# Performance work log

Measured on AMD Instinct MI355X. Metric: run time of the kernel, lower is better.

## Reference

```python
import jax, jax.numpy as jnp
import numpy as np

NB, M, FIN = 8, 32768, 32       # batch, mesh vertices, input features
RANK, FILT = 5, 32              # Chebyshev order, output filters
E = 262144                      # nnz of rescaled Laplacian (~8 per row)


def setup_inputs() -> dict:
    key = jax.random.key(0)
    ks = jax.random.split(key, 6)
    x = jax.random.normal(ks[0], (NB, M, FIN), dtype=jnp.float32)
    rows = jax.random.randint(ks[1], (E,), 0, M, dtype=jnp.int32)
    cols = jax.random.randint(ks[2], (E,), 0, M, dtype=jnp.int32)
    # rescaled-Laplacian values, roughly spectral-normalized
    vals = jax.random.normal(ks[3], (E,), dtype=jnp.float32) * np.float32(1.0 / np.sqrt(8.0))
    kernel = jax.random.normal(ks[4], (FIN * RANK, FILT), dtype=jnp.float32) * np.float32(0.05)
    bias = jnp.zeros((FILT,), dtype=jnp.float32)
    return {"x": x, "vals": vals, "kernel": kernel, "bias": bias, "rows": rows, "cols": cols}


def _spmm(rows, cols, vals, x0):
    # y[m, f, n] = sum_j L[m, j] * x0[j, f, n]   (COO SpMM via gather + segment_sum)
    g = vals[:, None, None] * x0[cols]           # [E, Fin, N]
    return jax.ops.segment_sum(g, rows, num_segments=x0.shape[0])


def reference(x, vals, kernel, bias, rows, cols):
    N, Mm, Fin = x.shape
    x0 = jnp.transpose(x, (1, 2, 0))             # [M, Fin, N]
    xs = [x0]
    x1 = x0
    if RANK > 1:
        x1 = _spmm(rows, cols, vals, x0)         # T_1 = L x
        xs.append(x1)
    for _ in range(2, RANK):                     # T_k = 2 L T_{k-1} - T_{k-2}
        x2 = 2.0 * _spmm(rows, cols, vals, x1) - x0
        xs.append(x2)
        x0, x1 = x1, x2
    xk = jnp.stack(xs, axis=0)                   # [K, M, Fin, N]
    xk = jnp.transpose(xk, (3, 1, 2, 0)).reshape(N * Mm, Fin * RANK)  # Fin-major, rank inner
    out = xk @ kernel + bias                     # [N*M, FILT]
    return out.reshape(N, Mm, FILT)
```

## Files before the change

kernel.cpp:

```cpp
#include <hip/hip_runtime.h>

#define M_VERT 32768
#define NBATCH 8
#define FIN 32
#define RANK 5
#define FILT 32
#define E_NNZ 262144
#define ROWLEN 256
#define EVROW 40

typedef short short8 __attribute__((ext_vector_type(8)));
typedef float f32x4 __attribute__((ext_vector_type(4)));

__device__ __forceinline__ float bfl(unsigned int u) {
    unsigned int x = u << 16; return __builtin_bit_cast(float, x);
}
__device__ __forceinline__ float bfh(unsigned int u) {
    unsigned int x = u & 0xffff0000u; return __builtin_bit_cast(float, x);
}
__device__ __forceinline__ unsigned int f2bf(float f) {
    unsigned int x = __builtin_bit_cast(unsigned int, f);
    return (x + 0x7fffu + ((x >> 16) & 1u)) >> 16;
}
__device__ __forceinline__ unsigned int pk(float a, float b) {
    return f2bf(a) | (f2bf(b) << 16);
}


__global__ void pack_kernel(const float* __restrict__ x, unsigned short* __restrict__ T0,
                            const int* __restrict__ rows, const int* __restrict__ cols,
                            const float* __restrict__ vals,
                            int* __restrict__ fill, int2* __restrict__ ev,
                            const float* __restrict__ W, unsigned short* __restrict__ Wb) {
    int tid = blockIdx.x * blockDim.x + threadIdx.x;
    int m = tid >> 5;
    int r = tid & 31;
    int n = r >> 2;
    int q = r & 3;
    const float* src = x + ((size_t)n * M_VERT + m) * FIN + q * 8;
    float4 v0 = *(const float4*)(src);
    float4 v1 = *(const float4*)(src + 4);
    uint4 u;
    u.x = pk(v0.x, v0.y); u.y = pk(v0.z, v0.w);
    u.z = pk(v1.x, v1.y); u.w = pk(v1.z, v1.w);
    *(uint4*)(T0 + (size_t)m * ROWLEN + n * FIN + q * 8) = u;

    if (tid < E_NNZ) {
        int rr = rows[tid];
        int pos = atomicAdd(&fill[rr], 1);
        if (pos < EVROW) {
            int2 p; p.x = cols[tid]; p.y = __builtin_bit_cast(int, vals[tid]);
            ev[rr * EVROW + pos] = p;
        }
    }

    if (tid < 640) {
        int lane = tid & 63;
        int kf = tid >> 6;
        int k = kf >> 1, ft = kf & 1;
        int f = ft * 16 + (lane & 15);
        int fin0 = (lane >> 4) * 8;
        unsigned short tmp[8];
#pragma unroll
        for (int j = 0; j < 8; ++j)
            tmp[j] = (unsigned short)f2bf(W[((fin0 + j) * RANK + k) * FILT + f]);
        uint4 uw;
        uw.x = (unsigned int)tmp[0] | ((unsigned int)tmp[1] << 16);
        uw.y = (unsigned int)tmp[2] | ((unsigned int)tmp[3] << 16);
        uw.z = (unsigned int)tmp[4] | ((unsigned int)tmp[5] << 16);
        uw.w = (unsigned int)tmp[6] | ((unsigned int)tmp[7] << 16);
        *(uint4*)(Wb + (size_t)tid * 8) = uw;
    }
}


__global__ __launch_bounds__(256) void spmm_kernel(const int* __restrict__ cnt,
                                                   const unsigned long long* __restrict__ ev,
                                                   const unsigned short* __restrict__ Tin,
                                                   const unsigned short* __restrict__ Tsub,
                                                   unsigned short* __restrict__ Tout, int cheb) {
    int w = threadIdx.x >> 6;
    int l = threadIdx.x & 63;
    int m = blockIdx.x * 4 + w;
    unsigned int coff = (unsigned int)l * 8u;
    int c = __builtin_amdgcn_readfirstlane(cnt[m]);
    int cp = (c + 7) & ~7;
    if (cp > EVROW) cp = EVROW;
    int s = m * EVROW;
    int e = s + cp;
    const char* tb = (const char*)Tin;
    float a0 = 0.f, a1 = 0.f, a2 = 0.f, a3 = 0.f;
    for (int j = s; j < e; j += 8) {
        unsigned long long ed[8];
#pragma unroll
        for (int i = 0; i < 8; ++i) ed[i] = ev[j + i];
        uint2 t[8];
#pragma unroll
        for (int i = 0; i < 8; ++i)
            t[i] = *(const uint2*)(tb + (((unsigned int)ed[i]) << 9) + coff);
#pragma unroll
        for (int i = 0; i < 8; ++i) {
            float v = __builtin_bit_cast(float, (unsigned int)(ed[i] >> 32));
            a0 += v * bfl(t[i].x); a1 += v * bfh(t[i].x);
            a2 += v * bfl(t[i].y); a3 += v * bfh(t[i].y);
        }
    }
    size_t moff = (size_t)m * 512 + coff;
    if (cheb) {
        unsigned long long o = __builtin_nontemporal_load(
            (const unsigned long long*)((const char*)Tsub + moff));
        unsigned int ox = (unsigned int)o, oy = (unsigned int)(o >> 32);
        a0 = 2.f * a0 - bfl(ox); a1 = 2.f * a1 - bfh(ox);
        a2 = 2.f * a2 - bfl(oy); a3 = 2.f * a3 - bfh(oy);
    }
    uint2 r;
    r.x = pk(a0, a1); r.y = pk(a2, a3);
    *(uint2*)((char*)Tout + moff) = r;
}


__global__ __launch_bounds__(256) void gemm_kernel(const unsigned short* __restrict__ T0,
                                                   const unsigned short* __restrict__ T1,
                                                   const unsigned short* __restrict__ T2,
                                                   const unsigned short* __restrict__ T3,
                                                   const unsigned short* __restrict__ T4,
                                                   const unsigned short* __restrict__ Wb,
                                                   const float* __restrict__ bias,
                                                   float* __restrict__ out) {
    int w = threadIdx.x >> 6;
    int l = threadIdx.x & 63;
    int n  = blockIdx.x & 7;
    int mb = blockIdx.x >> 3;
    int m0 = (mb * 4 + w) * 16;
    int lrow = l & 15;
    int quad = l >> 4;

    short8 bfrag[5][2];
#pragma unroll
    for (int kf = 0; kf < 10; ++kf)
        bfrag[kf >> 1][kf & 1] = *(const short8*)(Wb + ((size_t)kf * 64 + l) * 8);

    float b0 = bias[lrow];
    float b1 = bias[16 + lrow];

    const unsigned short* Ts[5] = {T0, T1, T2, T3, T4};
    size_t abase = (size_t)(m0 + lrow) * ROWLEN + quad * 8 + n * FIN;

    f32x4 c0 = {0.f, 0.f, 0.f, 0.f};
    f32x4 c1 = {0.f, 0.f, 0.f, 0.f};
#pragma unroll
    for (int k = 0; k < 5; ++k) {
        short8 a = *(const short8*)(Ts[k] + abase);
        c0 = __builtin_amdgcn_mfma_f32_16x16x32_bf16(a, bfrag[k][0], c0, 0, 0, 0);
        c1 = __builtin_amdgcn_mfma_f32_16x16x32_bf16(a, bfrag[k][1], c1, 0, 0, 0);
    }
    float* op = out + ((size_t)n * M_VERT + m0) * FILT;
#pragma unroll
    for (int r = 0; r < 4; ++r) {
        int orow = quad * 4 + r;
        __builtin_nontemporal_store(c0[r] + b0, &op[(size_t)orow * FILT + lrow]);
        __builtin_nontemporal_store(c1[r] + b1, &op[(size_t)orow * FILT + 16 + lrow]);
    }
}


extern "C" void kernel_launch(void* const* d_in, const int* in_sizes, int n_in,
                              void* d_out, int out_size, void* d_ws, size_t ws_size,
                              hipStream_t stream) {
    const float* x    = (const float*)d_in[0];
    const float* vals = (const float*)d_in[1];
    const float* W    = (const float*)d_in[2];
    const float* bias = (const float*)d_in[3];
    const int*   rows = (const int*)d_in[4];
    const int*   cols = (const int*)d_in[5];
    float* out = (float*)d_out;

    const size_t TSZ = (size_t)M_VERT * ROWLEN;
    unsigned short* T0 = (unsigned short*)d_ws;
    unsigned short* T1 = T0 + TSZ;
    unsigned short* T2 = T1 + TSZ;
    unsigned short* T3 = T2 + TSZ;
    unsigned short* T4 = T3 + TSZ;
    int*  fill = (int*)(T4 + TSZ);
    int2* ev   = (int2*)(fill + M_VERT);
    unsigned short* Wb = (unsigned short*)(ev + (size_t)M_VERT * EVROW);

    hipMemsetAsync(fill, 0, M_VERT * sizeof(int), stream);
    hipMemsetAsync(ev, 0, (size_t)M_VERT * EVROW * sizeof(int2), stream);
    pack_kernel<<<M_VERT * 32 / 256, 256, 0, stream>>>(x, T0, rows, cols, vals,
                                                       fill, ev, W, Wb);

    const unsigned long long* evq = (const unsigned long long*)ev;
    spmm_kernel<<<M_VERT / 4, 256, 0, stream>>>(fill, evq, T0, T0, T1, 0);
    spmm_kernel<<<M_VERT / 4, 256, 0, stream>>>(fill, evq, T1, T0, T2, 1);
    spmm_kernel<<<M_VERT / 4, 256, 0, stream>>>(fill, evq, T2, T1, T3, 1);
    spmm_kernel<<<M_VERT / 4, 256, 0, stream>>>(fill, evq, T3, T2, T4, 1);

    gemm_kernel<<<(M_VERT / 64) * 8, 256, 0, stream>>>(T0, T1, T2, T3, T4, Wb, bias, out);
}
```

Before: 231.4 us.

## Split Chebyshev tensors per batch and stage edge lists in LDS

Changes the T buffers from vertex-major rows holding all 8 batches [M][N*Fin] to batch-major [N][M][Fin]. Each SpMM block now handles 16 vertices for one batch, so each batch slice (2 MB of bf16) can stay cache-resident while neighbour rows are gathered. Edge lists are staged in shared memory once per block, and the loop runs to the exact count instead of padding to a multiple of 8, which lets the memset of the edge buffer be dropped. In exchange, each gather is now a 4-byte load per lane with 16-lane groups instead of an 8-byte load across a full wave, and edge lists are re-read once per batch.

```diff
diff --git a/kernel.cpp b/kernel.cpp
--- a/kernel.cpp
+++ b/kernel.cpp
@@ -33,17 +33,16 @@
                             int* __restrict__ fill, int2* __restrict__ ev,
                             const float* __restrict__ W, unsigned short* __restrict__ Wb) {
     int tid = blockIdx.x * blockDim.x + threadIdx.x;
-    int m = tid >> 5;
-    int r = tid & 31;
-    int n = r >> 2;
-    int q = r & 3;
+    int q = tid & 3;
+    int m = (tid >> 2) & (M_VERT - 1);
+    int n = tid >> 17;
     const float* src = x + ((size_t)n * M_VERT + m) * FIN + q * 8;
     float4 v0 = *(const float4*)(src);
     float4 v1 = *(const float4*)(src + 4);
     uint4 u;
     u.x = pk(v0.x, v0.y); u.y = pk(v0.z, v0.w);
     u.z = pk(v1.x, v1.y); u.w = pk(v1.z, v1.w);
-    *(uint4*)(T0 + (size_t)m * ROWLEN + n * FIN + q * 8) = u;
+    *(uint4*)(T0 + ((size_t)n * M_VERT + m) * 32 + q * 8) = u;
 
     if (tid < E_NNZ) {
         int rr = rows[tid];
@@ -79,43 +78,43 @@
                                                    const unsigned short* __restrict__ Tin,
                                                    const unsigned short* __restrict__ Tsub,
                                                    unsigned short* __restrict__ Tout, int cheb) {
-    int w = threadIdx.x >> 6;
-    int l = threadIdx.x & 63;
-    int m = blockIdx.x * 4 + w;
-    unsigned int coff = (unsigned int)l * 8u;
-    int c = __builtin_amdgcn_readfirstlane(cnt[m]);
-    int cp = (c + 7) & ~7;
-    if (cp > EVROW) cp = EVROW;
-    int s = m * EVROW;
-    int e = s + cp;
-    const char* tb = (const char*)Tin;
-    float a0 = 0.f, a1 = 0.f, a2 = 0.f, a3 = 0.f;
-    for (int j = s; j < e; j += 8) {
-        unsigned long long ed[8];
-#pragma unroll
-        for (int i = 0; i < 8; ++i) ed[i] = ev[j + i];
-        uint2 t[8];
-#pragma unroll
-        for (int i = 0; i < 8; ++i)
-            t[i] = *(const uint2*)(tb + (((unsigned int)ed[i]) << 9) + coff);
-#pragma unroll
-        for (int i = 0; i < 8; ++i) {
-            float v = __builtin_bit_cast(float, (unsigned int)(ed[i] >> 32));
-            a0 += v * bfl(t[i].x); a1 += v * bfh(t[i].x);
-            a2 += v * bfl(t[i].y); a3 += v * bfh(t[i].y);
-        }
+    __shared__ unsigned long long sev[16 * EVROW];
+    int n  = blockIdx.x & 7;
+    int vb = blockIdx.x >> 3;
+    int m0 = vb * 16;
+    int t  = threadIdx.x;
+
+    const unsigned long long* eb = ev + (size_t)m0 * EVROW;
+    for (int i = t; i < 16 * EVROW; i += 256)
+        sev[i] = __builtin_nontemporal_load(eb + i);
+
+    int g  = t >> 4;
+    int lq = t & 15;
+    int m  = m0 + g;
+    int c  = cnt[m];
+    if (c > EVROW) c = EVROW;
+    __syncthreads();
+
+    const char* sb = (const char*)Tin + ((size_t)n << 21);
+    unsigned int kof = (unsigned int)lq * 4u;
+    const unsigned long long* evg = sev + g * EVROW;
+    float a0 = 0.f, a1 = 0.f;
+    for (int j = 0; j < c; ++j) {
+        unsigned long long ed = evg[j];
+        unsigned int col = (unsigned int)ed;
+        float v = __builtin_bit_cast(float, (unsigned int)(ed >> 32));
+        unsigned int tv = *(const unsigned int*)(sb + (col << 6) + kof);
+        a0 += v * bfl(tv);
+        a1 += v * bfh(tv);
     }
-    size_t moff = (size_t)m * 512 + coff;
+    size_t moff = ((size_t)n << 21) + (((size_t)(unsigned int)m << 6) + kof);
     if (cheb) {
-        unsigned long long o = __builtin_nontemporal_load(
-            (const unsigned long long*)((const char*)Tsub + moff));
-        unsigned int ox = (unsigned int)o, oy = (unsigned int)(o >> 32);
-        a0 = 2.f * a0 - bfl(ox); a1 = 2.f * a1 - bfh(ox);
-        a2 = 2.f * a2 - bfl(oy); a3 = 2.f * a3 - bfh(oy);
+        unsigned int o = __builtin_nontemporal_load(
+            (const unsigned int*)((const char*)Tsub + moff));
+        a0 = 2.f * a0 - bfl(o);
+        a1 = 2.f * a1 - bfh(o);
     }
-    uint2 r;
-    r.x = pk(a0, a1); r.y = pk(a2, a3);
-    *(uint2*)((char*)Tout + moff) = r;
+    *(unsigned int*)((char*)Tout + moff) = pk(a0, a1);
 }
 
 
@@ -144,7 +143,7 @@
     float b1 = bias[16 + lrow];
 
     const unsigned short* Ts[5] = {T0, T1, T2, T3, T4};
-    size_t abase = (size_t)(m0 + lrow) * ROWLEN + quad * 8 + n * FIN;
+    size_t abase = ((size_t)n * M_VERT + (m0 + lrow)) * 32 + quad * 8;
 
     f32x4 c0 = {0.f, 0.f, 0.f, 0.f};
     f32x4 c1 = {0.f, 0.f, 0.f, 0.f};
@@ -186,15 +185,14 @@
     unsigned short* Wb = (unsigned short*)(ev + (size_t)M_VERT * EVROW);
 
     hipMemsetAsync(fill, 0, M_VERT * sizeof(int), stream);
-    hipMemsetAsync(ev, 0, (size_t)M_VERT * EVROW * sizeof(int2), stream);
     pack_kernel<<<M_VERT * 32 / 256, 256, 0, stream>>>(x, T0, rows, cols, vals,
                                                        fill, ev, W, Wb);
 
     const unsigned long long* evq = (const unsigned long long*)ev;
-    spmm_kernel<<<M_VERT / 4, 256, 0, stream>>>(fill, evq, T0, T0, T1, 0);
-    spmm_kernel<<<M_VERT / 4, 256, 0, stream>>>(fill, evq, T1, T0, T2, 1);
-    spmm_kernel<<<M_VERT / 4, 256, 0, stream>>>(fill, evq, T2, T1, T3, 1);
-    spmm_kernel<<<M_VERT / 4, 256, 0, stream>>>(fill, evq, T3, T2, T4, 1);
+    spmm_kernel<<<(M_VERT / 16) * 8, 256, 0, stream>>>(fill, evq, T0, T0, T1, 0);
+    spmm_kernel<<<(M_VERT / 16) * 8, 256, 0, stream>>>(fill, evq, T1, T0, T2, 1);
+    spmm_kernel<<<(M_VERT / 16) * 8, 256, 0, stream>>>(fill, evq, T2, T1, T3, 1);
+    spmm_kernel<<<(M_VERT / 16) * 8, 256, 0, stream>>>(fill, evq, T3, T2, T4, 1);
 
     gemm_kernel<<<(M_VERT / 64) * 8, 256, 0, stream>>>(T0, T1, T2, T3, T4, Wb, bias, out);
 }
```

Result: slower. 341.2 us (+47.4%).

## Fuse pack, SpMM chain and GEMM into one cooperative persistent kernel

Applied to the files above, without the earlier changes.

Replaces the two memsets and six separate kernel launches with a single cooperative kernel using grid-stride persistent loops and grid.sync between stages, sized from occupancy (up to 6 blocks per CU on 256 CUs). It aims to remove per-launch overhead and the tail drain between the dependent Chebyshev steps. In exchange, each stage runs on a capped persistent grid, and grid-wide barriers carry their own cost. The old multi-kernel path stays as a fallback if the cooperative launch fails.

```diff
diff --git a/kernel.cpp b/kernel.cpp
--- a/kernel.cpp
+++ b/kernel.cpp
@@ -1,4 +1,7 @@
 #include <hip/hip_runtime.h>
+#include <hip/hip_cooperative_groups.h>
+
+namespace cg = cooperative_groups;
 
 #define M_VERT 32768
 #define NBATCH 8
@@ -27,97 +30,204 @@
 }
 
 
-__global__ void pack_kernel(const float* __restrict__ x, unsigned short* __restrict__ T0,
-                            const int* __restrict__ rows, const int* __restrict__ cols,
-                            const float* __restrict__ vals,
-                            int* __restrict__ fill, int2* __restrict__ ev,
-                            const float* __restrict__ W, unsigned short* __restrict__ Wb) {
-    int tid = blockIdx.x * blockDim.x + threadIdx.x;
-    int m = tid >> 5;
-    int r = tid & 31;
-    int n = r >> 2;
-    int q = r & 3;
-    const float* src = x + ((size_t)n * M_VERT + m) * FIN + q * 8;
-    float4 v0 = *(const float4*)(src);
-    float4 v1 = *(const float4*)(src + 4);
-    uint4 u;
-    u.x = pk(v0.x, v0.y); u.y = pk(v0.z, v0.w);
-    u.z = pk(v1.x, v1.y); u.w = pk(v1.z, v1.w);
-    *(uint4*)(T0 + (size_t)m * ROWLEN + n * FIN + q * 8) = u;
-
-    if (tid < E_NNZ) {
-        int rr = rows[tid];
-        int pos = atomicAdd(&fill[rr], 1);
-        if (pos < EVROW) {
-            int2 p; p.x = cols[tid]; p.y = __builtin_bit_cast(int, vals[tid]);
-            ev[rr * EVROW + pos] = p;
-        }
-    }
-
-    if (tid < 640) {
-        int lane = tid & 63;
-        int kf = tid >> 6;
-        int k = kf >> 1, ft = kf & 1;
-        int f = ft * 16 + (lane & 15);
-        int fin0 = (lane >> 4) * 8;
-        unsigned short tmp[8];
-#pragma unroll
-        for (int j = 0; j < 8; ++j)
-            tmp[j] = (unsigned short)f2bf(W[((fin0 + j) * RANK + k) * FILT + f]);
-        uint4 uw;
-        uw.x = (unsigned int)tmp[0] | ((unsigned int)tmp[1] << 16);
-        uw.y = (unsigned int)tmp[2] | ((unsigned int)tmp[3] << 16);
-        uw.z = (unsigned int)tmp[4] | ((unsigned int)tmp[5] << 16);
-        uw.w = (unsigned int)tmp[6] | ((unsigned int)tmp[7] << 16);
-        *(uint4*)(Wb + (size_t)tid * 8) = uw;
-    }
-}
-
+__device__ __forceinline__ void pack_body(int G, const float* __restrict__ x,
+                                          unsigned short* __restrict__ T0,
+                                          const int* __restrict__ rows,
+                                          const int* __restrict__ cols,
+                                          const float* __restrict__ vals,
+                                          int* __restrict__ fill, int2* __restrict__ ev,
+                                          const float* __restrict__ W,
+                                          unsigned short* __restrict__ Wb) {
+    for (int tid = blockIdx.x * 256 + threadIdx.x; tid < M_VERT * 32; tid += G * 256) {
+        int m = tid >> 5;
+        int r = tid & 31;
+        int n = r >> 2;
+        int q = r & 3;
+        const float* src = x + ((size_t)n * M_VERT + m) * FIN + q * 8;
+        float4 v0 = *(const float4*)(src);
+        float4 v1 = *(const float4*)(src + 4);
+        uint4 u;
+        u.x = pk(v0.x, v0.y); u.y = pk(v0.z, v0.w);
+        u.z = pk(v1.x, v1.y); u.w = pk(v1.z, v1.w);
+        *(uint4*)(T0 + (size_t)m * ROWLEN + n * FIN + q * 8) = u;
+
+        if (tid < E_NNZ) {
+            int rr = rows[tid];
+            int pos = atomicAdd(&fill[rr], 1);
+            if (pos < EVROW) {
+                int2 p; p.x = cols[tid]; p.y = __builtin_bit_cast(int, vals[tid]);
+                ev[rr * EVROW + pos] = p;
+            }
+        }
+
+        if (tid < 640) {
+            int lane = tid & 63;
+            int kf = tid >> 6;
+            int k = kf >> 1, ft = kf & 1;
+            int f = ft * 16 + (lane & 15);
+            int fin0 = (lane >> 4) * 8;
+            unsigned short tmp[8];
+#pragma unroll
+            for (int j = 0; j < 8; ++j)
+                tmp[j] = (unsigned short)f2bf(W[((fin0 + j) * RANK + k) * FILT + f]);
+            uint4 uw;
+            uw.x = (unsigned int)tmp[0] | ((unsigned int)tmp[1] << 16);
+            uw.y = (unsigned int)tmp[2] | ((unsigned int)tmp[3] << 16);
+            uw.z = (unsigned int)tmp[4] | ((unsigned int)tmp[5] << 16);
+            uw.w = (unsigned int)tmp[6] | ((unsigned int)tmp[7] << 16);
+            *(uint4*)(Wb + (size_t)tid * 8) = uw;
+        }
+    }
+}
+
+__device__ __forceinline__ void spmm_body(int G, const int* __restrict__ cnt,
+                                          const unsigned long long* __restrict__ ev,
+                                          const unsigned short* __restrict__ Tin,
+                                          const unsigned short* __restrict__ Tsub,
+                                          unsigned short* __restrict__ Tout, int cheb) {
+    int w = threadIdx.x >> 6;
+    int l = threadIdx.x & 63;
+    unsigned int coff = (unsigned int)l * 8u;
+    const char* tb = (const char*)Tin;
+    for (int bv = blockIdx.x; bv < M_VERT / 4; bv += G) {
+        int m = bv * 4 + w;
+        int c = __builtin_amdgcn_readfirstlane(cnt[m]);
+        int cp = (c + 7) & ~7;
+        if (cp > EVROW) cp = EVROW;
+        int s = m * EVROW;
+        int e = s + cp;
+        float a0 = 0.f, a1 = 0.f, a2 = 0.f, a3 = 0.f;
+        for (int j = s; j < e; j += 8) {
+            unsigned long long ed[8];
+#pragma unroll
+            for (int i = 0; i < 8; ++i) ed[i] = ev[j + i];
+            uint2 t[8];
+#pragma unroll
+            for (int i = 0; i < 8; ++i)
+                t[i] = *(const uint2*)(tb + (((unsigned int)ed[i]) << 9) + coff);
+#pragma unroll
+            for (int i = 0; i < 8; ++i) {
+                float v = __builtin_bit_cast(float, (unsigned int)(ed[i] >> 32));
+                a0 += v * bfl(t[i].x); a1 += v * bfh(t[i].x);
+                a2 += v * bfl(t[i].y); a3 += v * bfh(t[i].y);
+            }
+        }
+        size_t moff = (size_t)m * 512 + coff;
+        if (cheb) {
+            unsigned long long o = __builtin_nontemporal_load(
+                (const unsigned long long*)((const char*)Tsub + moff));
+            unsigned int ox = (unsigned int)o, oy = (unsigned int)(o >> 32);
+            a0 = 2.f * a0 - bfl(ox); a1 = 2.f * a1 - bfh(ox);
+            a2 = 2.f * a2 - bfl(oy); a3 = 2.f * a3 - bfh(oy);
+        }
+        uint2 rr;
+        rr.x = pk(a0, a1); rr.y = pk(a2, a3);
+        *(uint2*)((char*)Tout + moff) = rr;
+    }
+}
+
+__device__ __forceinline__ void gemm_body(int G,
+                                          const unsigned short* __restrict__ T0,
+                                          const unsigned short* __restrict__ T1,
+                                          const unsigned short* __restrict__ T2,
+                                          const unsigned short* __restrict__ T3,
+                                          const unsigned short* __restrict__ T4,
+                                          const unsigned short* __restrict__ Wb,
+                                          const float* __restrict__ bias,
+                                          float* __restrict__ out) {
+    int w = threadIdx.x >> 6;
+    int l = threadIdx.x & 63;
+    int lrow = l & 15;
+    int quad = l >> 4;
+
+    short8 bfrag[5][2];
+#pragma unroll
+    for (int kf = 0; kf < 10; ++kf)
+        bfrag[kf >> 1][kf & 1] = *(const short8*)(Wb + ((size_t)kf * 64 + l) * 8);
+    float b0 = bias[lrow];
+    float b1 = bias[16 + lrow];
+    const unsigned short* Ts[5] = {T0, T1, T2, T3, T4};
+
+    for (int bv = blockIdx.x; bv < (M_VERT / 64) * 8; bv += G) {
+        int n  = bv & 7;
+        int mb = bv >> 3;
+        int m0 = (mb * 4 + w) * 16;
+        size_t abase = (size_t)(m0 + lrow) * ROWLEN + quad * 8 + n * FIN;
+        f32x4 c0 = {0.f, 0.f, 0.f, 0.f};
+        f32x4 c1 = {0.f, 0.f, 0.f, 0.f};
+#pragma unroll
+        for (int k = 0; k < 5; ++k) {
+            short8 a = *(const short8*)(Ts[k] + abase);
+            c0 = __builtin_amdgcn_mfma_f32_16x16x32_bf16(a, bfrag[k][0], c0, 0, 0, 0);
+            c1 = __builtin_amdgcn_mfma_f32_16x16x32_bf16(a, bfrag[k][1], c1, 0, 0, 0);
+        }
+        float* op = out + ((size_t)n * M_VERT + m0) * FILT;
+#pragma unroll
+        for (int r = 0; r < 4; ++r) {
+            int orow = quad * 4 + r;
+            __builtin_nontemporal_store(c0[r] + b0, &op[(size_t)orow * FILT + lrow]);
+            __builtin_nontemporal_store(c1[r] + b1, &op[(size_t)orow * FILT + 16 + lrow]);
+        }
+    }
+}
+
+
+__global__ __launch_bounds__(256) void fused_kernel(const float* __restrict__ x,
+                                                    const int* __restrict__ rows,
+                                                    const int* __restrict__ cols,
+                                                    const float* __restrict__ vals,
+                                                    const float* __restrict__ W,
+                                                    const float* __restrict__ bias,
+                                                    float* __restrict__ out,
+                                                    unsigned short* T0, unsigned short* T1,
+                                                    unsigned short* T2, unsigned short* T3,
+                                                    unsigned short* T4,
+                                                    int* fill, int2* ev,
+                                                    unsigned short* Wb) {
+    cg::grid_group grid = cg::this_grid();
+    const int G = gridDim.x;
+
+    {
+        int4* z = (int4*)fill;
+        const int total = (M_VERT * 4 + M_VERT * EVROW * 8) / 16;
+        int4 zero = {0, 0, 0, 0};
+        for (int i = blockIdx.x * 256 + threadIdx.x; i < total; i += G * 256)
+            z[i] = zero;
+    }
+    grid.sync();
+
+    pack_body(G, x, T0, rows, cols, vals, fill, ev, W, Wb);
+    grid.sync();
+
+    const unsigned long long* evq = (const unsigned long long*)ev;
+    spmm_body(G, fill, evq, T0, T0, T1, 0); grid.sync();
+    spmm_body(G, fill, evq, T1, T0, T2, 1); grid.sync();
+    spmm_body(G, fill, evq, T2, T1, T3, 1); grid.sync();
+    spmm_body(G, fill, evq, T3, T2, T4, 1); grid.sync();
+
+    gemm_body(G, T0, T1, T2, T3, T4, Wb, bias, out);
+}
+
+
+__global__ __launch_bounds__(256) void pack_kernel(const float* __restrict__ x,
+                                                   unsigned short* __restrict__ T0,
+                                                   const int* __restrict__ rows,
+                                                   const int* __restrict__ cols,
+                                                   const float* __restrict__ vals,
+                                                   int* __restrict__ fill,
+                                                   int2* __restrict__ ev,
+                                                   const float* __restrict__ W,
+                                                   unsigned short* __restrict__ Wb) {
+    pack_body(gridDim.x, x, T0, rows, cols, vals, fill, ev, W, Wb);
+}
 
 __global__ __launch_bounds__(256) void spmm_kernel(const int* __restrict__ cnt,
                                                    const unsigned long long* __restrict__ ev,
                                                    const unsigned short* __restrict__ Tin,
                                                    const unsigned short* __restrict__ Tsub,
                                                    unsigned short* __restrict__ Tout, int cheb) {
-    int w = threadIdx.x >> 6;
-    int l = threadIdx.x & 63;
-    int m = blockIdx.x * 4 + w;
-    unsigned int coff = (unsigned int)l * 8u;
-    int c = __builtin_amdgcn_readfirstlane(cnt[m]);
-    int cp = (c + 7) & ~7;
-    if (cp > EVROW) cp = EVROW;
-    int s = m * EVROW;
-    int e = s + cp;
-    const char* tb = (const char*)Tin;
-    float a0 = 0.f, a1 = 0.f, a2 = 0.f, a3 = 0.f;
-    for (int j = s; j < e; j += 8) {
-        unsigned long long ed[8];
-#pragma unroll
-        for (int i = 0; i < 8; ++i) ed[i] = ev[j + i];
-        uint2 t[8];
-#pragma unroll
-        for (int i = 0; i < 8; ++i)
-            t[i] = *(const uint2*)(tb + (((unsigned int)ed[i]) << 9) + coff);
-#pragma unroll
-        for (int i = 0; i < 8; ++i) {
-            float v = __builtin_bit_cast(float, (unsigned int)(ed[i] >> 32));
-            a0 += v * bfl(t[i].x); a1 += v * bfh(t[i].x);
-            a2 += v * bfl(t[i].y); a3 += v * bfh(t[i].y);
-        }
-    }
-    size_t moff = (size_t)m * 512 + coff;
-    if (cheb) {
-        unsigned long long o = __builtin_nontemporal_load(
-            (const unsigned long long*)((const char*)Tsub + moff));
-        unsigned int ox = (unsigned int)o, oy = (unsigned int)(o >> 32);
-        a0 = 2.f * a0 - bfl(ox); a1 = 2.f * a1 - bfh(ox);
-        a2 = 2.f * a2 - bfl(oy); a3 = 2.f * a3 - bfh(oy);
-    }
-    uint2 r;
-    r.x = pk(a0, a1); r.y = pk(a2, a3);
-    *(uint2*)((char*)Tout + moff) = r;
-}
-
+    spmm_body(gridDim.x, cnt, ev, Tin, Tsub, Tout, cheb);
+}
 
 __global__ __launch_bounds__(256) void gemm_kernel(const unsigned short* __restrict__ T0,
                                                    const unsigned short* __restrict__ T1,
@@ -127,40 +237,7 @@
                                                    const unsigned short* __restrict__ Wb,
                                                    const float* __restrict__ bias,
                                                    float* __restrict__ out) {
-    int w = threadIdx.x >> 6;
-    int l = threadIdx.x & 63;
-    int n  = blockIdx.x & 7;
-    int mb = blockIdx.x >> 3;
-    int m0 = (mb * 4 + w) * 16;
-    int lrow = l & 15;
-    int quad = l >> 4;
-
-    short8 bfrag[5][2];
-#pragma unroll
-    for (int kf = 0; kf < 10; ++kf)
-        bfrag[kf >> 1][kf & 1] = *(const short8*)(Wb + ((size_t)kf * 64 + l) * 8);
-
-    float b0 = bias[lrow];
-    float b1 = bias[16 + lrow];
-
-    const unsigned short* Ts[5] = {T0, T1, T2, T3, T4};
-    size_t abase = (size_t)(m0 + lrow) * ROWLEN + quad * 8 + n * FIN;
-
-    f32x4 c0 = {0.f, 0.f, 0.f, 0.f};
-    f32x4 c1 = {0.f, 0.f, 0.f, 0.f};
-#pragma unroll
-    for (int k = 0; k < 5; ++k) {
-        short8 a = *(const short8*)(Ts[k] + abase);
-        c0 = __builtin_amdgcn_mfma_f32_16x16x32_bf16(a, bfrag[k][0], c0, 0, 0, 0);
-        c1 = __builtin_amdgcn_mfma_f32_16x16x32_bf16(a, bfrag[k][1], c1, 0, 0, 0);
-    }
-    float* op = out + ((size_t)n * M_VERT + m0) * FILT;
-#pragma unroll
-    for (int r = 0; r < 4; ++r) {
-        int orow = quad * 4 + r;
-        __builtin_nontemporal_store(c0[r] + b0, &op[(size_t)orow * FILT + lrow]);
-        __builtin_nontemporal_store(c1[r] + b1, &op[(size_t)orow * FILT + 16 + lrow]);
-    }
+    gemm_body(gridDim.x, T0, T1, T2, T3, T4, Wb, bias, out);
 }
 
 
@@ -185,16 +262,37 @@
     int2* ev   = (int2*)(fill + M_VERT);
     unsigned short* Wb = (unsigned short*)(ev + (size_t)M_VERT * EVROW);
 
-    hipMemsetAsync(fill, 0, M_VERT * sizeof(int), stream);
-    hipMemsetAsync(ev, 0, (size_t)M_VERT * EVROW * sizeof(int2), stream);
-    pack_kernel<<<M_VERT * 32 / 256, 256, 0, stream>>>(x, T0, rows, cols, vals,
-                                                       fill, ev, W, Wb);
-
-    const unsigned long long* evq = (const unsigned long long*)ev;
-    spmm_kernel<<<M_VERT / 4, 256, 0, stream>>>(fill, evq, T0, T0, T1, 0);
-    spmm_kernel<<<M_VERT / 4, 256, 0, stream>>>(fill, evq, T1, T0, T2, 1);
-    spmm_kernel<<<M_VERT / 4, 256, 0, stream>>>(fill, evq, T2, T1, T3, 1);
-    spmm_kernel<<<M_VERT / 4, 256, 0, stream>>>(fill, evq, T3, T2, T4, 1);
-
-    gemm_kernel<<<(M_VERT / 64) * 8, 256, 0, stream>>>(T0, T1, T2, T3, T4, Wb, bias, out);
-}
+    static int blocksPerCU = 0;
+    if (blocksPerCU == 0) {
+        int nb = 0;
+        hipError_t qe = hipOccupancyMaxActiveBlocksPerMultiprocessor(
+            &nb, (const void*)fused_kernel, 256, 0);
+        blocksPerCU = (qe == hipSuccess && nb > 0) ? nb : -1;
+    }
+
+    bool launched = false;
+    if (blocksPerCU > 0) {
+        int bpc = blocksPerCU > 6 ? 6 : blocksPerCU;
+        dim3 grid(bpc * 256), block(256);
+        void* args[] = {(void*)&x, (void*)&rows, (void*)&cols, (void*)&vals,
+                        (void*)&W, (void*)&bias, (void*)&out,
+                        (void*)&T0, (void*)&T1, (void*)&T2, (void*)&T3, (void*)&T4,
+                        (void*)&fill, (void*)&ev, (void*)&Wb};
+        hipError_t le = hipLaunchCooperativeKernel((const void*)fused_kernel,
+                                                   grid, block, args, 0, stream);
+        launched = (le == hipSuccess);
+    }
+
+    if (!launched) {
+        hipMemsetAsync(fill, 0, M_VERT * sizeof(int), stream);
+        hipMemsetAsync(ev, 0, (size_t)M_VERT * EVROW * sizeof(int2), stream);
+        pack_kernel<<<M_VERT * 32 / 256, 256, 0, stream>>>(x, T0, rows, cols, vals,
+                                                           fill, ev, W, Wb);
+        const unsigned long long* evq = (const unsigned long long*)ev;
+        spmm_kernel<<<M_VERT / 4, 256, 0, stream>>>(fill, evq, T0, T0, T1, 0);
+        spmm_kernel<<<M_VERT / 4, 256, 0, stream>>>(fill, evq, T1, T0, T2, 1);
+        spmm_kernel<<<M_VERT / 4, 256, 0, stream>>>(fill, evq, T2, T1, T3, 1);
+        spmm_kernel<<<M_VERT / 4, 256, 0, stream>>>(fill, evq, T3, T2, T4, 1);
+        gemm_kernel<<<(M_VERT / 64) * 8, 256, 0, stream>>>(T0, T1, T2, T3, T4, Wb, bias, out);
+    }
+}
```

Measured after the change: 786.5 us. +239.8%, slower.

## Fuse last SpMM step with output GEMM via LDS and drop ev memset

Applied to the files above, without the earlier changes.

The final Chebyshev SpMM is merged into the GEMM kernel: each 1024-thread block computes T4 for 64 vertices into swizzled shared memory, then runs the MFMA GEMM reading T0-T3 from global memory and T4 from LDS. This removes the T4 global round-trip and one kernel launch. SpMM loops now handle the tail with masked loads, so the 21 MB memset of the edge buffer is no longer needed. The cost is lower parallelism in the fused SpMM (one block per 64 rows) and weight fragments reloaded per tile.

```diff
diff --git a/kernel.cpp b/kernel.cpp
--- a/kernel.cpp
+++ b/kernel.cpp
@@ -11,6 +11,7 @@
 
 typedef short short8 __attribute__((ext_vector_type(8)));
 typedef float f32x4 __attribute__((ext_vector_type(4)));
+typedef unsigned long long u64;
 
 __device__ __forceinline__ float bfl(unsigned int u) {
     unsigned int x = u << 16; return __builtin_bit_cast(float, x);
@@ -75,7 +76,7 @@
 
 
 __global__ __launch_bounds__(256) void spmm_kernel(const int* __restrict__ cnt,
-                                                   const unsigned long long* __restrict__ ev,
+                                                   const u64* __restrict__ ev,
                                                    const unsigned short* __restrict__ Tin,
                                                    const unsigned short* __restrict__ Tsub,
                                                    unsigned short* __restrict__ Tout, int cheb) {
@@ -84,16 +85,16 @@
     int m = blockIdx.x * 4 + w;
     unsigned int coff = (unsigned int)l * 8u;
     int c = __builtin_amdgcn_readfirstlane(cnt[m]);
-    int cp = (c + 7) & ~7;
-    if (cp > EVROW) cp = EVROW;
+    if (c > EVROW) c = EVROW;
     int s = m * EVROW;
-    int e = s + cp;
+    int cf = c & ~7;
     const char* tb = (const char*)Tin;
     float a0 = 0.f, a1 = 0.f, a2 = 0.f, a3 = 0.f;
-    for (int j = s; j < e; j += 8) {
-        unsigned long long ed[8];
-#pragma unroll
-        for (int i = 0; i < 8; ++i) ed[i] = ev[j + i];
+    int j = 0;
+    for (; j < cf; j += 8) {
+        u64 ed[8];
+#pragma unroll
+        for (int i = 0; i < 8; ++i) ed[i] = ev[s + j + i];
         uint2 t[8];
 #pragma unroll
         for (int i = 0; i < 8; ++i)
@@ -105,61 +106,151 @@
             a2 += v * bfl(t[i].y); a3 += v * bfh(t[i].y);
         }
     }
+    if (j < c) {
+        int rem = c - j;
+        u64 ed[8];
+#pragma unroll
+        for (int i = 0; i < 8; ++i) ed[i] = ev[s + j + i];
+        unsigned int cm[8]; float vm[8];
+#pragma unroll
+        for (int i = 0; i < 8; ++i) {
+            bool ok = i < rem;
+            cm[i] = ok ? (unsigned int)ed[i] : 0u;
+            vm[i] = ok ? __builtin_bit_cast(float, (unsigned int)(ed[i] >> 32)) : 0.f;
+        }
+        uint2 t[8];
+#pragma unroll
+        for (int i = 0; i < 8; ++i)
+            t[i] = *(const uint2*)(tb + (cm[i] << 9) + coff);
+#pragma unroll
+        for (int i = 0; i < 8; ++i) {
+            a0 += vm[i] * bfl(t[i].x); a1 += vm[i] * bfh(t[i].x);
+            a2 += vm[i] * bfl(t[i].y); a3 += vm[i] * bfh(t[i].y);
+        }
+    }
     size_t moff = (size_t)m * 512 + coff;
     if (cheb) {
-        unsigned long long o = __builtin_nontemporal_load(
-            (const unsigned long long*)((const char*)Tsub + moff));
+        u64 o = __builtin_nontemporal_load((const u64*)((const char*)Tsub + moff));
         unsigned int ox = (unsigned int)o, oy = (unsigned int)(o >> 32);
         a0 = 2.f * a0 - bfl(ox); a1 = 2.f * a1 - bfh(ox);
         a2 = 2.f * a2 - bfl(oy); a3 = 2.f * a3 - bfh(oy);
     }
-    uint2 r;
-    r.x = pk(a0, a1); r.y = pk(a2, a3);
-    *(uint2*)((char*)Tout + moff) = r;
-}
-
-
-__global__ __launch_bounds__(256) void gemm_kernel(const unsigned short* __restrict__ T0,
-                                                   const unsigned short* __restrict__ T1,
-                                                   const unsigned short* __restrict__ T2,
-                                                   const unsigned short* __restrict__ T3,
-                                                   const unsigned short* __restrict__ T4,
-                                                   const unsigned short* __restrict__ Wb,
-                                                   const float* __restrict__ bias,
-                                                   float* __restrict__ out) {
+    uint2 rr;
+    rr.x = pk(a0, a1); rr.y = pk(a2, a3);
+    *(uint2*)((char*)Tout + moff) = rr;
+}
+
+
+__global__ __launch_bounds__(1024, 8) void spmm4_gemm_kernel(
+        const int* __restrict__ cnt, const u64* __restrict__ ev,
+        const unsigned short* __restrict__ T0, const unsigned short* __restrict__ T1,
+        const unsigned short* __restrict__ T2, const unsigned short* __restrict__ T3,
+        const unsigned short* __restrict__ Wb, const float* __restrict__ bias,
+        float* __restrict__ out) {
+    __shared__ unsigned short sT4[64 * 256];
     int w = threadIdx.x >> 6;
     int l = threadIdx.x & 63;
-    int n  = blockIdx.x & 7;
-    int mb = blockIdx.x >> 3;
-    int m0 = (mb * 4 + w) * 16;
+    int mb0 = blockIdx.x * 64;
+    unsigned int coff = (unsigned int)l * 8u;
+    const char* tb = (const char*)T3;
+
+    for (int vi = 0; vi < 4; ++vi) {
+        int lr = w * 4 + vi;
+        int m = mb0 + lr;
+        int c = __builtin_amdgcn_readfirstlane(cnt[m]);
+        if (c > EVROW) c = EVROW;
+        int s = m * EVROW;
+        int cf = c & ~7;
+        float a0 = 0.f, a1 = 0.f, a2 = 0.f, a3 = 0.f;
+        int j = 0;
+        for (; j < cf; j += 8) {
+            u64 ed[8];
+#pragma unroll
+            for (int i = 0; i < 8; ++i) ed[i] = ev[s + j + i];
+            uint2 t[8];
+#pragma unroll
+            for (int i = 0; i < 8; ++i)
+                t[i] = *(const uint2*)(tb + (((unsigned int)ed[i]) << 9) + coff);
+#pragma unroll
+            for (int i = 0; i < 8; ++i) {
+                float v = __builtin_bit_cast(float, (unsigned int)(ed[i] >> 32));
+                a0 += v * bfl(t[i].x); a1 += v * bfh(t[i].x);
+                a2 += v * bfl(t[i].y); a3 += v * bfh(t[i].y);
+            }
+        }
+        if (j < c) {
+            int rem = c - j;
+            u64 ed[8];
+#pragma unroll
+            for (int i = 0; i < 8; ++i) ed[i] = ev[s + j + i];
+            unsigned int cm[8]; float vm[8];
+#pragma unroll
+            for (int i = 0; i < 8; ++i) {
+                bool ok = i < rem;
+                cm[i] = ok ? (unsigned int)ed[i] : 0u;
+                vm[i] = ok ? __builtin_bit_cast(float, (unsigned int)(ed[i] >> 32)) : 0.f;
+            }
+            uint2 t[8];
+#pragma unroll
+            for (int i = 0; i < 8; ++i)
+                t[i] = *(const uint2*)(tb + (cm[i] << 9) + coff);
+#pragma unroll
+            for (int i = 0; i < 8; ++i) {
+                a0 += vm[i] * bfl(t[i].x); a1 += vm[i] * bfh(t[i].x);
+                a2 += vm[i] * bfl(t[i].y); a3 += vm[i] * bfh(t[i].y);
+            }
+        }
+        size_t moff = (size_t)(mb0 + lr) * 512 + coff;
+        u64 o = __builtin_nontemporal_load((const u64*)((const char*)T2 + moff));
+        unsigned int ox = (unsigned int)o, oy = (unsigned int)(o >> 32);
+        a0 = 2.f * a0 - bfl(ox); a1 = 2.f * a1 - bfh(ox);
+        a2 = 2.f * a2 - bfl(oy); a3 = 2.f * a3 - bfh(oy);
+        uint2 rr;
+        rr.x = pk(a0, a1); rr.y = pk(a2, a3);
+        unsigned int swz = coff ^ (((unsigned int)lr & 7u) << 4);
+        *(uint2*)((char*)sT4 + lr * 512 + swz) = rr;
+    }
+    __syncthreads();
+
     int lrow = l & 15;
     int quad = l >> 4;
-
-    short8 bfrag[5][2];
-#pragma unroll
-    for (int kf = 0; kf < 10; ++kf)
-        bfrag[kf >> 1][kf & 1] = *(const short8*)(Wb + ((size_t)kf * 64 + l) * 8);
-
     float b0 = bias[lrow];
     float b1 = bias[16 + lrow];
-
-    const unsigned short* Ts[5] = {T0, T1, T2, T3, T4};
-    size_t abase = (size_t)(m0 + lrow) * ROWLEN + quad * 8 + n * FIN;
-
-    f32x4 c0 = {0.f, 0.f, 0.f, 0.f};
-    f32x4 c1 = {0.f, 0.f, 0.f, 0.f};
-#pragma unroll
-    for (int k = 0; k < 5; ++k) {
-        short8 a = *(const short8*)(Ts[k] + abase);
-        c0 = __builtin_amdgcn_mfma_f32_16x16x32_bf16(a, bfrag[k][0], c0, 0, 0, 0);
-        c1 = __builtin_amdgcn_mfma_f32_16x16x32_bf16(a, bfrag[k][1], c1, 0, 0, 0);
-    }
-    float* op = out + ((size_t)n * M_VERT + m0) * FILT;
-#pragma unroll
-    for (int r = 0; r < 4; ++r) {
-        int orow = quad * 4 + r;
-        __builtin_nontemporal_store(c0[r] + b0, &op[(size_t)orow * FILT + lrow]);
-        __builtin_nontemporal_store(c1[r] + b1, &op[(size_t)orow * FILT + 16 + lrow]);
+    const unsigned short* Ts[4] = {T0, T1, T2, T3};
+
+    for (int tt = w; tt < 32; tt += 16) {
+        int n  = tt & 7;
+        int rg = tt >> 3;
+        int m0l = rg * 16;
+        int m0  = mb0 + m0l;
+        size_t abase = (size_t)(m0 + lrow) * ROWLEN + quad * 8 + n * FIN;
+        f32x4 c0 = {0.f, 0.f, 0.f, 0.f};
+        f32x4 c1 = {0.f, 0.f, 0.f, 0.f};
+#pragma unroll
+        for (int k = 0; k < 4; ++k) {
+            short8 a  = *(const short8*)(Ts[k] + abase);
+            short8 f0 = *(const short8*)(Wb + ((size_t)(k * 2 + 0) * 64 + l) * 8);
+            short8 f1 = *(const short8*)(Wb + ((size_t)(k * 2 + 1) * 64 + l) * 8);
+            c0 = __builtin_amdgcn_mfma_f32_16x16x32_bf16(a, f0, c0, 0, 0, 0);
+            c1 = __builtin_amdgcn_mfma_f32_16x16x32_bf16(a, f1, c1, 0, 0, 0);
+        }
+        {
+            int rloc = m0l + lrow;
+            unsigned int boff = ((unsigned int)(n * 64 + quad * 16))
+                              ^ (((unsigned int)rloc & 7u) << 4);
+            short8 a  = *(const short8*)((const char*)sT4 + rloc * 512 + boff);
+            short8 f0 = *(const short8*)(Wb + ((size_t)(8) * 64 + l) * 8);
+            short8 f1 = *(const short8*)(Wb + ((size_t)(9) * 64 + l) * 8);
+            c0 = __builtin_amdgcn_mfma_f32_16x16x32_bf16(a, f0, c0, 0, 0, 0);
+            c1 = __builtin_amdgcn_mfma_f32_16x16x32_bf16(a, f1, c1, 0, 0, 0);
+        }
+        float* op = out + ((size_t)n * M_VERT + m0) * FILT;
+#pragma unroll
+        for (int r = 0; r < 4; ++r) {
+            int orow = quad * 4 + r;
+            __builtin_nontemporal_store(c0[r] + b0, &op[(size_t)orow * FILT + lrow]);
+            __builtin_nontemporal_store(c1[r] + b1, &op[(size_t)orow * FILT + 16 + lrow]);
+        }
     }
 }
 
@@ -180,21 +271,19 @@
     unsigned short* T1 = T0 + TSZ;
     unsigned short* T2 = T1 + TSZ;
     unsigned short* T3 = T2 + TSZ;
-    unsigned short* T4 = T3 + TSZ;
-    int*  fill = (int*)(T4 + TSZ);
+    int*  fill = (int*)(T3 + TSZ);
     int2* ev   = (int2*)(fill + M_VERT);
     unsigned short* Wb = (unsigned short*)(ev + (size_t)M_VERT * EVROW);
 
     hipMemsetAsync(fill, 0, M_VERT * sizeof(int), stream);
-    hipMemsetAsync(ev, 0, (size_t)M_VERT * EVROW * sizeof(int2), stream);
     pack_kernel<<<M_VERT * 32 / 256, 256, 0, stream>>>(x, T0, rows, cols, vals,
                                                        fill, ev, W, Wb);
 
-    const unsigned long long* evq = (const unsigned long long*)ev;
+    const u64* evq = (const u64*)ev;
     spmm_kernel<<<M_VERT / 4, 256, 0, stream>>>(fill, evq, T0, T0, T1, 0);
     spmm_kernel<<<M_VERT / 4, 256, 0, stream>>>(fill, evq, T1, T0, T2, 1);
     spmm_kernel<<<M_VERT / 4, 256, 0, stream>>>(fill, evq, T2, T1, T3, 1);
-    spmm_kernel<<<M_VERT / 4, 256, 0, stream>>>(fill, evq, T3, T2, T4, 1);
-
-    gemm_kernel<<<(M_VERT / 64) * 8, 256, 0, stream>>>(T0, T1, T2, T3, T4, Wb, bias, out);
-}
+
+    spmm4_gemm_kernel<<<M_VERT / 64, 1024, 0, stream>>>(fill, evq, T0, T1, T2, T3,
+                                                        Wb, bias, out);
+}
```

Measured after the change: 228.4 us. About the same (-1.3%).
